# Performance work log

Hardware: AMD Instinct MI355X
Metric: run time of the kernel (lower is better)

Reference implementation:

```python
import jax, jax.numpy as jnp
import numpy as np

B, H, W = 32, 56, 56
C_IN, C_OUT, GROUPS, K = 256, 256, 32, 3
EPS = 1e-5


def setup_inputs() -> dict:
    key = jax.random.key(0)
    k1, k2 = jax.random.split(key, 2)
    x = jax.random.normal(k1, (B, H, W, C_IN), dtype=jnp.float32)
    # HWIO grouped-conv kernel: I = C_IN // GROUPS = 8; equivalent to the
    # concatenation of the 32 per-group [3,3,8,8] Conv2d kernels along O.
    w = jax.random.normal(k2, (K, K, C_IN // GROUPS, C_OUT), dtype=jnp.float32) * 0.05
    b = jnp.zeros((C_OUT,), dtype=jnp.float32)
    gamma = jnp.ones((C_OUT,), dtype=jnp.float32)
    beta = jnp.zeros((C_OUT,), dtype=jnp.float32)
    return {"x": x, "w": w, "b": b, "gamma": gamma, "beta": beta}


def reference(x, w, b, gamma, beta):
    # Grouped conv: same math as tf.split -> per-group Conv2d -> tf.concat,
    # expressed as one native grouped convolution (feature_group_count).
    y = jax.lax.conv_general_dilated(
        x, w,
        window_strides=(1, 1),
        padding="SAME",
        dimension_numbers=("NHWC", "HWIO", "NHWC"),
        feature_group_count=GROUPS,
    ) + b  # [B,H,W,C_OUT]
    # BatchNorm (training forward: batch statistics over N,H,W per channel)
    mean = jnp.mean(y, axis=(0, 1, 2))
    var = jnp.var(y, axis=(0, 1, 2))
    y = (y - mean) * jax.lax.rsqrt(var + EPS) * gamma + beta
    # Act('relu')
    return jax.nn.relu(y)
```

## Files before the change

kernel.cpp:

```cpp
#include <hip/hip_runtime.h>
#include <hip/hip_bf16.h>

#define BB 32
#define HH 56
#define WW 56
#define CC 256
#define NPIX (BB*HH*WW)
#define EPS 1e-5f

typedef short bf16x8 __attribute__((ext_vector_type(8)));
typedef float f32x4  __attribute__((ext_vector_type(4)));

__device__ __forceinline__ unsigned short f2bf(float f) {
    __hip_bfloat16 h = __float2bfloat16(f);
    return *reinterpret_cast<unsigned short*>(&h);
}


__global__ void k0_zero(float* stats) { stats[threadIdx.x] = 0.f; }

__global__ __launch_bounds__(256) void k1_conv(
    const float* __restrict__ x, const float* __restrict__ wgt,
    __hip_bfloat16* __restrict__ y, float* __restrict__ stats)
{
    __shared__ unsigned short xt[10*58*24];
    __shared__ unsigned short wb[16*160];
    __shared__ float bsum[16], bsq[16];

    const int gp = blockIdx.x;
    const int hb = blockIdx.y;
    const int b  = blockIdx.z;
    const int t  = threadIdx.x;
    const int h0 = hb * 8;

    if (t < 16) { bsum[t] = 0.f; bsq[t] = 0.f; }

    float4 v[10];
    int    off[10];
    #pragma unroll
    for (int j = 0; j < 10; ++j) {
        const int i   = j*256 + t;
        const int ci4 = i & 3;
        const int cq  = i >> 2;
        const int row = cq / 58;
        const int col = cq - row*58;
        const int hh  = h0 - 1 + row;
        const int wc  = col - 1;
        off[j] = (row*58 + col)*24 + ci4*4;
        v[j] = make_float4(0.f, 0.f, 0.f, 0.f);
        if (i < 2320 && (unsigned)hh < HH && (unsigned)wc < WW)
            v[j] = *(const float4*)(x + (((size_t)(b*HH + hh)*WW + wc)*CC + gp*16 + ci4*4));
    }
    {
        const int n  = t >> 4;
        const int k0 = t & 15;
        #pragma unroll
        for (int j = 0; j < 10; ++j) {
            const int kk  = k0 + j*16;
            const int g   = (kk >= 80);
            const int r   = kk - g*80;
            const int tap = r >> 3, ci = r & 7;
            unsigned short val = 0;
            if (tap < 9 && (n >> 3) == g)
                val = f2bf(wgt[(tap*8 + ci)*CC + gp*16 + n]);
            wb[n*160 + kk] = val;
        }
    }
    #pragma unroll
    for (int j = 0; j < 10; ++j) {
        if (j*256 + t < 2320) {
            ushort4 s;
            s.x = f2bf(v[j].x); s.y = f2bf(v[j].y);
            s.z = f2bf(v[j].z); s.w = f2bf(v[j].w);
            *(ushort4*)(xt + off[j]) = s;
        }
    }
    __syncthreads();

    const int lane = t & 63;
    const int rp   = t >> 6;
    const int n    = lane & 15;
    const int q    = lane >> 4;
    const int m    = lane & 15;
    const int rowr = rp*2 + (m >> 3);
    const int colb = m & 7;

    bf16x8 bfrag[5];
    #pragma unroll
    for (int s = 0; s < 5; ++s)
        bfrag[s] = *(const bf16x8*)(wb + n*160 + s*32 + q*8);

    int aoff[5];
    #pragma unroll
    for (int s = 0; s < 5; ++s) {
        int o  = s*4 + q;
        int g  = (o >= 10);
        int tp = o - g*10;
        if (tp == 9) tp = 0;
        int dh = tp / 3, dw = tp - dh*3;
        aoff[s] = ((rowr + dh)*58 + colb + dw)*24 + g*8;
    }

    const int hq = q >> 1;
    const int wq = (q & 1) * 4;
    float lsum = 0.f, lsq = 0.f;

    #pragma unroll 2
    for (int ct = 0; ct < 7; ++ct) {
        f32x4 acc = {0.f, 0.f, 0.f, 0.f};
        #pragma unroll
        for (int s = 0; s < 5; ++s) {
            bf16x8 af = *(const bf16x8*)(xt + aoff[s] + ct*192);
            acc = __builtin_amdgcn_mfma_f32_16x16x32_bf16(af, bfrag[s], acc, 0, 0, 0);
        }
        const int h = h0 + rp*2 + hq;
        const size_t base = (((size_t)(b*HH + h))*WW + ct*8 + wq)*CC + gp*16 + n;
        #pragma unroll
        for (int i = 0; i < 4; ++i) {
            float vv = acc[i];
            y[base + (size_t)i*CC] = __float2bfloat16(vv);
            lsum += vv;
            lsq  += vv * vv;
        }
    }

    atomicAdd(&bsum[n], lsum);
    atomicAdd(&bsq[n],  lsq);
    __syncthreads();
    if (t < 16) {
        atomicAdd(&stats[gp*16 + t],       bsum[t]);
        atomicAdd(&stats[256 + gp*16 + t], bsq[t]);
    }
}

__global__ void k2_finalize(const float* __restrict__ stats,
                            const float* __restrict__ gamma,
                            const float* __restrict__ beta,
                            float* __restrict__ ss)
{
    int c = threadIdx.x;
    float inv_n = 1.f / (float)NPIX;
    float mean = stats[c] * inv_n;
    float var  = stats[256 + c] * inv_n - mean * mean;
    float scale = gamma[c] * rsqrtf(var + EPS);
    ss[c]       = scale;
    ss[256 + c] = beta[c] - mean * scale;
}

__global__ __launch_bounds__(256) void k3_norm(
    const __hip_bfloat16* __restrict__ y, const float* __restrict__ ss,
    float* __restrict__ out)
{
    const int t   = threadIdx.x;
    const int oct = t & 31;
    const int pr  = t >> 5;
    const int c0  = oct * 8;

    float4 sc0 = *(const float4*)(ss + c0);
    float4 sc1 = *(const float4*)(ss + c0 + 4);
    float4 sh0 = *(const float4*)(ss + 256 + c0);
    float4 sh1 = *(const float4*)(ss + 256 + c0 + 4);

    const uint4* yv = (const uint4*)y;
    float4* ov = (float4*)out;
    const int px0 = blockIdx.x * 32 + pr;

    uint4 d[4];
    #pragma unroll
    for (int i = 0; i < 4; ++i)
        d[i] = yv[(size_t)(px0 + i*8)*32 + oct];

    #pragma unroll
    for (int i = 0; i < 4; ++i) {
        const int px = px0 + i*8;
        float f0 = __uint_as_float((d[i].x & 0xffffu) << 16);
        float f1 = __uint_as_float(d[i].x & 0xffff0000u);
        float f2 = __uint_as_float((d[i].y & 0xffffu) << 16);
        float f3 = __uint_as_float(d[i].y & 0xffff0000u);
        float f4 = __uint_as_float((d[i].z & 0xffffu) << 16);
        float f5 = __uint_as_float(d[i].z & 0xffff0000u);
        float f6 = __uint_as_float((d[i].w & 0xffffu) << 16);
        float f7 = __uint_as_float(d[i].w & 0xffff0000u);

        float4 o0, o1;
        o0.x = fmaxf(0.f, f0 * sc0.x + sh0.x);
        o0.y = fmaxf(0.f, f1 * sc0.y + sh0.y);
        o0.z = fmaxf(0.f, f2 * sc0.z + sh0.z);
        o0.w = fmaxf(0.f, f3 * sc0.w + sh0.w);
        o1.x = fmaxf(0.f, f4 * sc1.x + sh1.x);
        o1.y = fmaxf(0.f, f5 * sc1.y + sh1.y);
        o1.z = fmaxf(0.f, f6 * sc1.z + sh1.z);
        o1.w = fmaxf(0.f, f7 * sc1.w + sh1.w);

        ov[(size_t)px*64 + oct*2]     = o0;
        ov[(size_t)px*64 + oct*2 + 1] = o1;
    }
}

extern "C" void kernel_launch(void* const* d_in, const int* in_sizes, int n_in,
                              void* d_out, int out_size, void* d_ws, size_t ws_size,
                              hipStream_t stream) {
    const float* x     = (const float*)d_in[0];
    const float* wgt   = (const float*)d_in[1];
    const float* gamma = (const float*)d_in[3];
    const float* beta  = (const float*)d_in[4];
    float* out = (float*)d_out;

    float* stats = (float*)d_ws;
    float* ss    = (float*)((char*)d_ws + 2048);
    __hip_bfloat16* y = (__hip_bfloat16*)((char*)d_ws + 4096);

    k0_zero<<<1, 512, 0, stream>>>(stats);
    k1_conv<<<dim3(16, 7, BB), 256, 0, stream>>>(x, wgt, y, stats);
    k2_finalize<<<1, 256, 0, stream>>>(stats, gamma, beta, ss);
    k3_norm<<<NPIX/32, 256, 0, stream>>>(y, ss, out);
}
```

Baseline: 250.0 us.

## Stream conv input tiles via LDS DMA double-buffering across persistent row loop

The conv kernel now runs one block per (group pair, batch) and loops over the seven 8-row bands. It double-buffers fp32 input tiles in LDS using global_load_lds DMA, so the next band's loads overlap MFMA work on the current band. The fp32-to-bf16 conversion moves into the A-fragment read path through a rounding add and byte-permute. Separately, the zero kernel becomes hipMemsetAsync, the norm kernel handles half as many pixels per block, and outputs use nontemporal stores. This trades fewer and larger blocks (less parallelism, with a launch-bounds occupancy hint) and more LDS traffic, since tiles are kept in fp32, for hidden load latency.

```diff
diff --git a/kernel.cpp b/kernel.cpp
--- a/kernel.cpp
+++ b/kernel.cpp
@@ -10,55 +10,44 @@
 
 typedef short bf16x8 __attribute__((ext_vector_type(8)));
 typedef float f32x4  __attribute__((ext_vector_type(4)));
+typedef unsigned int u32;
 
 __device__ __forceinline__ unsigned short f2bf(float f) {
     __hip_bfloat16 h = __float2bfloat16(f);
     return *reinterpret_cast<unsigned short*>(&h);
 }
 
-
-__global__ void k0_zero(float* stats) { stats[threadIdx.x] = 0.f; }
-
-__global__ __launch_bounds__(256) void k1_conv(
+__device__ __forceinline__ void dma16(const float* g, void* l) {
+    __builtin_amdgcn_global_load_lds(
+        (const __attribute__((address_space(1))) void*)g,
+        (__attribute__((address_space(3))) void*)l, 16, 0, 0);
+}
+
+
+__global__ __launch_bounds__(256, 2) void k1_conv(
     const float* __restrict__ x, const float* __restrict__ wgt,
     __hip_bfloat16* __restrict__ y, float* __restrict__ stats)
 {
-    __shared__ unsigned short xt[10*58*24];
+    __shared__ float xb[2][4*580*4];
     __shared__ unsigned short wb[16*160];
     __shared__ float bsum[16], bsq[16];
 
-    const int gp = blockIdx.x;
-    const int hb = blockIdx.y;
-    const int b  = blockIdx.z;
-    const int t  = threadIdx.x;
-    const int h0 = hb * 8;
+    const int gp   = blockIdx.x;
+    const int b    = blockIdx.y;
+    const int t    = threadIdx.x;
+    const int lane = t & 63;
+    const int wv   = t >> 6;
 
     if (t < 16) { bsum[t] = 0.f; bsq[t] = 0.f; }
 
-    float4 v[10];
-    int    off[10];
-    #pragma unroll
-    for (int j = 0; j < 10; ++j) {
-        const int i   = j*256 + t;
-        const int ci4 = i & 3;
-        const int cq  = i >> 2;
-        const int row = cq / 58;
-        const int col = cq - row*58;
-        const int hh  = h0 - 1 + row;
-        const int wc  = col - 1;
-        off[j] = (row*58 + col)*24 + ci4*4;
-        v[j] = make_float4(0.f, 0.f, 0.f, 0.f);
-        if (i < 2320 && (unsigned)hh < HH && (unsigned)wc < WW)
-            v[j] = *(const float4*)(x + (((size_t)(b*HH + hh)*WW + wc)*CC + gp*16 + ci4*4));
-    }
     {
         const int n  = t >> 4;
         const int k0 = t & 15;
         #pragma unroll
         for (int j = 0; j < 10; ++j) {
-            const int kk  = k0 + j*16;
-            const int g   = (kk >= 80);
-            const int r   = kk - g*80;
+            const int kk = k0 + j*16;
+            const int g  = (kk >= 80);
+            const int r  = kk - g*80;
             const int tap = r >> 3, ci = r & 7;
             unsigned short val = 0;
             if (tap < 9 && (n >> 3) == g)
@@ -66,31 +55,55 @@
             wb[n*160 + kk] = val;
         }
     }
+
+    if (t < 160) {
+        int bi = (t >= 80);
+        int i  = t - bi*80;
+        int plane = i / 20;
+        int rem = i - plane*20;
+        int row = rem >> 1;
+        int col = (rem & 1) ? 57 : 0;
+        *(f32x4*)&xb[bi][(plane*580 + row*58 + col)*4] = (f32x4){0.f,0.f,0.f,0.f};
+    }
+
+    const int nj = (wv < 3) ? 10 : 7;
+    int goff[10];
+    int mmid = 0, mfirst = 0, mlast = 0;
     #pragma unroll
     for (int j = 0; j < 10; ++j) {
-        if (j*256 + t < 2320) {
-            ushort4 s;
-            s.x = f2bf(v[j].x); s.y = f2bf(v[j].y);
-            s.z = f2bf(v[j].z); s.w = f2bf(v[j].w);
-            *(ushort4*)(xt + off[j]) = s;
-        }
-    }
-    __syncthreads();
-
-    const int lane = t & 63;
-    const int rp   = t >> 6;
+        int I = wv*10 + j;
+        int slot = I*64 + lane;
+        int plane = slot / 580;
+        int rem  = slot - plane*580;
+        int row  = rem / 58;
+        int col  = rem - row*58;
+        goff[j] = ((row - 1)*WW + (col - 1))*CC + plane*4;
+        bool colok = (plane < 4) && (col >= 1) && (col <= 56);
+        if (colok) {
+            mmid |= 1 << j;
+            if (row >= 1) mfirst |= 1 << j;
+            if (row <= 8) mlast  |= 1 << j;
+        }
+    }
+    const int xbase  = (b*HH*WW)*CC + gp*16;
+    const int wvu10  = __builtin_amdgcn_readfirstlane(wv) * 10;
+
+    #pragma unroll
+    for (int j = 0; j < 10; ++j)
+        if (j < nj && ((mfirst >> j) & 1))
+            dma16(x + xbase + goff[j], (char*)&xb[0][0] + (wvu10 + j)*1024);
+    if (t < 224) {
+        int plane = t / 56;
+        int col = t - plane*56 + 1;
+        *(f32x4*)&xb[0][(plane*580 + col)*4] = (f32x4){0.f,0.f,0.f,0.f};
+    }
+
     const int n    = lane & 15;
     const int q    = lane >> 4;
-    const int m    = lane & 15;
-    const int rowr = rp*2 + (m >> 3);
-    const int colb = m & 7;
-
-    bf16x8 bfrag[5];
-    #pragma unroll
-    for (int s = 0; s < 5; ++s)
-        bfrag[s] = *(const bf16x8*)(wb + n*160 + s*32 + q*8);
-
-    int aoff[5];
+    const int mm   = lane & 15;
+    const int rowr = wv*2 + (mm >> 3);
+    const int colb = mm & 7;
+    int aoffB[5];
     #pragma unroll
     for (int s = 0; s < 5; ++s) {
         int o  = s*4 + q;
@@ -98,29 +111,70 @@
         int tp = o - g*10;
         if (tp == 9) tp = 0;
         int dh = tp / 3, dw = tp - dh*3;
-        aoff[s] = ((rowr + dh)*58 + colb + dw)*24 + g*8;
-    }
-
+        aoffB[s] = ((2*g*580) + (rowr + dh)*58 + (colb + dw)) * 16;
+    }
     const int hq = q >> 1;
     const int wq = (q & 1) * 4;
     float lsum = 0.f, lsq = 0.f;
 
-    #pragma unroll 2
-    for (int ct = 0; ct < 7; ++ct) {
-        f32x4 acc = {0.f, 0.f, 0.f, 0.f};
-        #pragma unroll
-        for (int s = 0; s < 5; ++s) {
-            bf16x8 af = *(const bf16x8*)(xt + aoff[s] + ct*192);
-            acc = __builtin_amdgcn_mfma_f32_16x16x32_bf16(af, bfrag[s], acc, 0, 0, 0);
-        }
-        const int h = h0 + rp*2 + hq;
-        const size_t base = (((size_t)(b*HH + h))*WW + ct*8 + wq)*CC + gp*16 + n;
-        #pragma unroll
-        for (int i = 0; i < 4; ++i) {
-            float vv = acc[i];
-            y[base + (size_t)i*CC] = __float2bfloat16(vv);
-            lsum += vv;
-            lsq  += vv * vv;
+    __syncthreads();
+    bf16x8 bfrag[5];
+    #pragma unroll
+    for (int s = 0; s < 5; ++s)
+        bfrag[s] = *(const bf16x8*)(wb + n*160 + s*32 + q*8);
+
+    for (int hb = 0; hb < 7; ++hb) {
+        __syncthreads();
+
+        if (hb < 6) {
+            float* dst = &xb[(hb + 1) & 1][0];
+            const int msk = (hb + 1 == 6) ? mlast : mmid;
+            const int go  = xbase + (hb + 1)*8*WW*CC;
+            #pragma unroll
+            for (int j = 0; j < 10; ++j)
+                if (j < nj && ((msk >> j) & 1))
+                    dma16(x + go + goff[j], (char*)dst + (wvu10 + j)*1024);
+            if (hb + 1 == 6 && t < 224) {
+                int plane = t / 56;
+                int col = t - plane*56 + 1;
+                *(f32x4*)&dst[(plane*580 + 9*58 + col)*4] = (f32x4){0.f,0.f,0.f,0.f};
+            }
+        }
+
+        const float* src = &xb[hb & 1][0];
+        #pragma unroll 2
+        for (int ct = 0; ct < 7; ++ct) {
+            f32x4 acc = {0.f,0.f,0.f,0.f};
+            #pragma unroll
+            for (int s = 0; s < 5; ++s) {
+                const char* p = (const char*)src + aoffB[s] + ct*128;
+                f32x4 lo = *(const f32x4*)p;
+                f32x4 hi = *(const f32x4*)(p + 9280);
+                u32 a0 = __float_as_uint(lo[0]) + 0x8000u;
+                u32 a1 = __float_as_uint(lo[1]) + 0x8000u;
+                u32 a2 = __float_as_uint(lo[2]) + 0x8000u;
+                u32 a3 = __float_as_uint(lo[3]) + 0x8000u;
+                u32 a4 = __float_as_uint(hi[0]) + 0x8000u;
+                u32 a5 = __float_as_uint(hi[1]) + 0x8000u;
+                u32 a6 = __float_as_uint(hi[2]) + 0x8000u;
+                u32 a7 = __float_as_uint(hi[3]) + 0x8000u;
+                uint4 pk;
+                pk.x = __builtin_amdgcn_perm(a1, a0, 0x07060302u);
+                pk.y = __builtin_amdgcn_perm(a3, a2, 0x07060302u);
+                pk.z = __builtin_amdgcn_perm(a5, a4, 0x07060302u);
+                pk.w = __builtin_amdgcn_perm(a7, a6, 0x07060302u);
+                bf16x8 af = __builtin_bit_cast(bf16x8, pk);
+                acc = __builtin_amdgcn_mfma_f32_16x16x32_bf16(af, bfrag[s], acc, 0, 0, 0);
+            }
+            const int h = hb*8 + wv*2 + hq;
+            const size_t base = (((size_t)(b*HH + h))*WW + ct*8 + wq)*CC + gp*16 + n;
+            #pragma unroll
+            for (int i = 0; i < 4; ++i) {
+                float vv = acc[i];
+                y[base + (size_t)i*CC] = __float2bfloat16(vv);
+                lsum += vv;
+                lsq  += vv * vv;
+            }
         }
     }
 
@@ -162,16 +216,15 @@
     float4 sh1 = *(const float4*)(ss + 256 + c0 + 4);
 
     const uint4* yv = (const uint4*)y;
-    float4* ov = (float4*)out;
-    const int px0 = blockIdx.x * 32 + pr;
-
-    uint4 d[4];
-    #pragma unroll
-    for (int i = 0; i < 4; ++i)
+    const int px0 = blockIdx.x * 16 + pr;
+
+    uint4 d[2];
+    #pragma unroll
+    for (int i = 0; i < 2; ++i)
         d[i] = yv[(size_t)(px0 + i*8)*32 + oct];
 
     #pragma unroll
-    for (int i = 0; i < 4; ++i) {
+    for (int i = 0; i < 2; ++i) {
         const int px = px0 + i*8;
         float f0 = __uint_as_float((d[i].x & 0xffffu) << 16);
         float f1 = __uint_as_float(d[i].x & 0xffff0000u);
@@ -182,18 +235,19 @@
         float f6 = __uint_as_float((d[i].w & 0xffffu) << 16);
         float f7 = __uint_as_float(d[i].w & 0xffff0000u);
 
-        float4 o0, o1;
-        o0.x = fmaxf(0.f, f0 * sc0.x + sh0.x);
-        o0.y = fmaxf(0.f, f1 * sc0.y + sh0.y);
-        o0.z = fmaxf(0.f, f2 * sc0.z + sh0.z);
-        o0.w = fmaxf(0.f, f3 * sc0.w + sh0.w);
-        o1.x = fmaxf(0.f, f4 * sc1.x + sh1.x);
-        o1.y = fmaxf(0.f, f5 * sc1.y + sh1.y);
-        o1.z = fmaxf(0.f, f6 * sc1.z + sh1.z);
-        o1.w = fmaxf(0.f, f7 * sc1.w + sh1.w);
-
-        ov[(size_t)px*64 + oct*2]     = o0;
-        ov[(size_t)px*64 + oct*2 + 1] = o1;
+        f32x4 o0, o1;
+        o0[0] = fmaxf(0.f, f0 * sc0.x + sh0.x);
+        o0[1] = fmaxf(0.f, f1 * sc0.y + sh0.y);
+        o0[2] = fmaxf(0.f, f2 * sc0.z + sh0.z);
+        o0[3] = fmaxf(0.f, f3 * sc0.w + sh0.w);
+        o1[0] = fmaxf(0.f, f4 * sc1.x + sh1.x);
+        o1[1] = fmaxf(0.f, f5 * sc1.y + sh1.y);
+        o1[2] = fmaxf(0.f, f6 * sc1.z + sh1.z);
+        o1[3] = fmaxf(0.f, f7 * sc1.w + sh1.w);
+
+        f32x4* op = (f32x4*)out + (size_t)px*64 + oct*2;
+        __builtin_nontemporal_store(o0, op);
+        __builtin_nontemporal_store(o1, op + 1);
     }
 }
 
@@ -210,8 +264,8 @@
     float* ss    = (float*)((char*)d_ws + 2048);
     __hip_bfloat16* y = (__hip_bfloat16*)((char*)d_ws + 4096);
 
-    k0_zero<<<1, 512, 0, stream>>>(stats);
-    k1_conv<<<dim3(16, 7, BB), 256, 0, stream>>>(x, wgt, y, stats);
+    hipMemsetAsync(stats, 0, 2048, stream);
+    k1_conv<<<dim3(16, BB), 256, 0, stream>>>(x, wgt, y, stats);
     k2_finalize<<<1, 256, 0, stream>>>(stats, gamma, beta, ss);
-    k3_norm<<<NPIX/32, 256, 0, stream>>>(y, ss, out);
-}
+    k3_norm<<<NPIX/16, 256, 0, stream>>>(y, ss, out);
+}
```

Result: slower. 289.5 us (+15.8%).
